# Kernel tuning notes

Measured on AMD Instinct MI355X. Metric: run time of the kernel, lower is better.

Reference implementation:

```python
import jax, jax.numpy as jnp
import numpy as np

EMBED = 8192      # DYNAMIC(2048) + STATIC(6144)
U0, U1 = 1024, 256  # units
EGO = 3
NUM_HEAD = 6
ACTION = 2
MEAN_SCALE = 5.0
INIT_STD = 5.0
MIN_STD = 1e-4
BATCH = 8192


def setup_inputs() -> dict:
    key = jax.random.key(0)
    ks = jax.random.split(key, 10)
    s = lambda fan_in: 1.0 / np.sqrt(fan_in)
    x = jax.random.normal(ks[0], (BATCH, EMBED), dtype=jnp.float32)
    # command head index in [0, 6) == RoadOption.value - 1
    command = jax.random.randint(ks[1], (BATCH,), 0, NUM_HEAD, dtype=jnp.int32)
    ego_state = jax.random.normal(ks[2], (BATCH, EGO), dtype=jnp.float32)
    # shared trunk fc: Linear(EMBED -> U0)
    fc_W = jax.random.uniform(ks[3], (EMBED, U0), jnp.float32, -s(EMBED), s(EMBED))
    fc_b = jax.random.uniform(ks[4], (U0,), jnp.float32, -s(EMBED), s(EMBED))
    # per-head MLP: Linear(U0+EGO -> U1) -> ReLU -> Linear(U1 -> 2*ACTION)
    cin = U0 + EGO
    W1 = jax.random.uniform(ks[5], (NUM_HEAD, cin, U1), jnp.float32, -s(cin), s(cin))
    b1 = jax.random.uniform(ks[6], (NUM_HEAD, U1), jnp.float32, -s(cin), s(cin))
    W2 = jax.random.uniform(ks[7], (NUM_HEAD, U1, 2 * ACTION), jnp.float32, -s(U1), s(U1))
    b2 = jax.random.uniform(ks[8], (NUM_HEAD, 2 * ACTION), jnp.float32, -s(U1), s(U1))
    return {"x": x, "command": command, "ego_state": ego_state,
            "fc_W": fc_W, "fc_b": fc_b, "W1": W1, "b1": b1, "W2": W2, "b2": b2}


def reference(x, command, ego_state, fc_W, fc_b, W1, b1, W2, b2):
    # shared trunk: Linear + ReLU, then concat ego state -> [B, U0+EGO]
    h = jax.nn.relu(x @ fc_W + fc_b)
    h = jnp.concatenate([h, ego_state], axis=-1)
    # routed heads: compute all 6 small heads densely, then select per sample
    # (faithful math; an optimized kernel would gather->grouped GEMM->scatter)
    h1 = jax.nn.relu(jnp.einsum('bi,hio->bho', h, W1) + b1)          # [B, H, U1]
    h2 = jnp.einsum('bhi,hio->bho', h1, W2) + b2                      # [B, H, 2A]
    sel = jnp.take_along_axis(h2, command[:, None, None].astype(jnp.int32), axis=1)
    out = sel[:, 0, :]                                                # [B, 2A]
    mean, std = jnp.split(out, 2, axis=-1)
    mean = MEAN_SCALE * jnp.tanh(mean / MEAN_SCALE)
    raw_init_std = np.float32(np.log(np.exp(INIT_STD) - 1.0))
    std = jax.nn.softplus(std + raw_init_std) + MIN_STD
    # distribution parameters (pre TanhBijector Normal params)
    return jnp.concatenate([mean, std], axis=-1)
```

## Files before the change

kernel.cpp:

```cpp
#include <hip/hip_runtime.h>
#include <stdint.h>

typedef short bf16x8 __attribute__((ext_vector_type(8)));
typedef float f32x4 __attribute__((ext_vector_type(4)));

#define BATCH 8192
#define EMBED 8192
#define U0    1024
#define U1    256
#define NHEAD 6

__device__ __forceinline__ unsigned short f2bf(float f) {
  union { float f; unsigned int u; } v; v.f = f;
  unsigned int u = v.u;
  unsigned int r = u + 0x7FFFu + ((u >> 16) & 1u);
  return (unsigned short)(r >> 16);
}
__device__ __forceinline__ unsigned int pk2(float lo, float hi) {
  return (unsigned int)f2bf(lo) | ((unsigned int)f2bf(hi) << 16);
}
__device__ __forceinline__ void async_copy16(const void* g, void* l) {
  __builtin_amdgcn_global_load_lds((const __attribute__((address_space(1))) void*)g,
                                   (__attribute__((address_space(3))) void*)l, 16, 0, 0);
}

__global__ void cvt_x_kernel(const float* __restrict__ x, unsigned short* __restrict__ xb) {
  long i = ((long)blockIdx.x * 256 + threadIdx.x) * 8;
  float4 a = *(const float4*)(x + i);
  float4 b = *(const float4*)(x + i + 4);
  uint4 r;
  r.x = pk2(a.x, a.y); r.y = pk2(a.z, a.w);
  r.z = pk2(b.x, b.y); r.w = pk2(b.z, b.w);
  *(uint4*)(xb + i) = r;
}

__global__ void transpose_cvt_kernel(const float* __restrict__ in, unsigned short* __restrict__ out,
                                     int R, int C, long in_z, long out_z) {
  __shared__ unsigned short tile[64][65];
  const float* inp = in + (long)blockIdx.z * in_z;
  unsigned short* outp = out + (long)blockIdx.z * out_z;
  int r0 = blockIdx.x * 64;
  int c0 = blockIdx.y * 64;
  int lc = threadIdx.x & 63;
  int lr = threadIdx.x >> 6;
#pragma unroll
  for (int i = 0; i < 16; i++) {
    int r = lr + i * 4;
    tile[r][lc] = f2bf(inp[(long)(r0 + r) * C + (c0 + lc)]);
  }
  __syncthreads();
#pragma unroll
  for (int i = 0; i < 16; i++) {
    int c = lr + i * 4;
    outp[(long)(c0 + c) * R + (r0 + lc)] = tile[lc][c];
  }
}

__global__ void bucket_kernel(const int* __restrict__ cmd, int* __restrict__ idxlist,
                              int* __restrict__ meta) {
  __shared__ int cnt[NHEAD], cur[NHEAD], off[NHEAD + 1];
  int tid = threadIdx.x;
  int lane = tid & 63;
  if (tid < NHEAD) cnt[tid] = 0;
  __syncthreads();
  for (int b = tid; b < BATCH; b += 1024) {
    int c = cmd[b];
#pragma unroll
    for (int h2 = 0; h2 < NHEAD; h2++) {
      unsigned long long m = __ballot(c == h2);
      if (lane == 0 && m) atomicAdd(&cnt[h2], __popcll(m));
    }
  }
  __syncthreads();
  if (tid == 0) {
    int s = 0;
    for (int h2 = 0; h2 < NHEAD; h2++) { off[h2] = s; s += cnt[h2]; }
    off[NHEAD] = s;
  }
  __syncthreads();
  if (tid < NHEAD) cur[tid] = off[tid];
  if (tid <= NHEAD) meta[tid] = off[tid];
  __syncthreads();
  for (int b = tid; b < BATCH; b += 1024) {
    int c = cmd[b];
#pragma unroll
    for (int h2 = 0; h2 < NHEAD; h2++) {
      unsigned long long m = __ballot(c == h2);
      int mypos = __popcll(m & ((1ull << lane) - 1ull));
      int base = 0;
      if (lane == 0 && m) base = atomicAdd(&cur[h2], __popcll(m));
      base = __shfl(base, 0);
      if (c == h2) idxlist[base + mypos] = b;
    }
  }
}

__global__ __launch_bounds__(256, 4) void gemm_kernel(const unsigned short* __restrict__ xb,
                                                      const unsigned short* __restrict__ wt,
                                                      const float* __restrict__ fc_b,
                                                      unsigned short* __restrict__ h) {
  __shared__ uint4 As[1024];
  __shared__ uint4 Bs[512];
  int tid  = threadIdx.x;
  int lane = tid & 63;
  int wave = tid >> 6;
  int wm = wave >> 1, wn = wave & 1;
  int m0 = blockIdx.x * 128;
  int n0 = blockIdx.y * 64;
  int l15 = lane & 15, lq = lane >> 4;

  long asrc[4];
#pragma unroll
  for (int j = 0; j < 4; j++) {
    int c = wave * 4 + j;
    int cwm = c >> 3, cks = (c >> 2) & 1, cmi = c & 3;
    asrc[j] = (long)(m0 + cwm * 64 + cmi * 16 + l15) * EMBED + cks * 32 + lq * 8;
  }
  long bsrc[2];
#pragma unroll
  for (int j = 0; j < 2; j++) {
    int c = wave * 2 + j;
    int cwn = c >> 2, cks = (c >> 1) & 1, cni = c & 1;
    bsrc[j] = (long)(n0 + cwn * 32 + cni * 16 + l15) * EMBED + cks * 32 + lq * 8;
  }

  f32x4 zero = {0.f, 0.f, 0.f, 0.f};
  f32x4 acc[4][2];
#pragma unroll
  for (int mi = 0; mi < 4; mi++)
#pragma unroll
    for (int ni = 0; ni < 2; ni++) acc[mi][ni] = zero;

  for (int k0 = 0; k0 < EMBED; k0 += 64) {
    __syncthreads();
#pragma unroll
    for (int j = 0; j < 4; j++) {
      int c = wave * 4 + j;
      async_copy16(xb + asrc[j] + k0, &As[c * 64 + lane]);
    }
#pragma unroll
    for (int j = 0; j < 2; j++) {
      int c = wave * 2 + j;
      async_copy16(wt + bsrc[j] + k0, &Bs[c * 64 + lane]);
    }
    __syncthreads();
#pragma unroll
    for (int ks = 0; ks < 2; ks++) {
      bf16x8 af[4], bfr[2];
#pragma unroll
      for (int mi = 0; mi < 4; mi++) af[mi] = *(const bf16x8*)&As[((wm * 2 + ks) * 4 + mi) * 64 + lane];
#pragma unroll
      for (int ni = 0; ni < 2; ni++) bfr[ni] = *(const bf16x8*)&Bs[((wn * 2 + ks) * 2 + ni) * 64 + lane];
#pragma unroll
      for (int mi = 0; mi < 4; mi++)
#pragma unroll
        for (int ni = 0; ni < 2; ni++)
          acc[mi][ni] = __builtin_amdgcn_mfma_f32_16x16x32_bf16(af[mi], bfr[ni], acc[mi][ni], 0, 0, 0);
    }
  }

#pragma unroll
  for (int ni = 0; ni < 2; ni++) {
    int col = n0 + wn * 32 + ni * 16 + l15;
    float bias = fc_b[col];
#pragma unroll
    for (int mi = 0; mi < 4; mi++) {
      int rbase = m0 + wm * 64 + mi * 16 + lq * 4;
#pragma unroll
      for (int r = 0; r < 4; r++) {
        float v = acc[mi][ni][r] + bias;
        v = v > 0.f ? v : 0.f;
        h[(long)(rbase + r) * U0 + col] = f2bf(v);
      }
    }
  }
}

__global__ __launch_bounds__(256) void head_kernel(const unsigned short* __restrict__ h,
                                                   const unsigned short* __restrict__ w1t,
                                                   const float* __restrict__ W1,
                                                   const float* __restrict__ b1,
                                                   const float* __restrict__ W2,
                                                   const float* __restrict__ b2,
                                                   const float* __restrict__ ego,
                                                   const int* __restrict__ idxlist,
                                                   const int* __restrict__ meta,
                                                   float* __restrict__ out) {
  int hd = blockIdx.y;
  int off = meta[hd];
  int cnt = meta[hd + 1] - off;
  int t0 = blockIdx.x * 32;
  if (t0 >= cnt) return;

  __shared__ int ridx[32];
  __shared__ float h1s[32][257];
  int tid = threadIdx.x;
  if (tid < 32) {
    int i = t0 + tid;
    ridx[tid] = idxlist[off + (i < cnt ? i : 0)];
  }
  __syncthreads();

  int lane = tid & 63, wave = tid >> 6;
  int l15 = lane & 15, lq = lane >> 4;

  long abase[2];
#pragma unroll
  for (int mi = 0; mi < 2; mi++) abase[mi] = (long)ridx[mi * 16 + l15] * U0 + lq * 8;
  long bbase[4];
#pragma unroll
  for (int ni = 0; ni < 4; ni++)
    bbase[ni] = (long)(hd * 256 + wave * 64 + ni * 16 + l15) * 1024 + lq * 8;

  f32x4 zero = {0.f, 0.f, 0.f, 0.f};
  f32x4 acc[2][4];
#pragma unroll
  for (int mi = 0; mi < 2; mi++)
#pragma unroll
    for (int ni = 0; ni < 4; ni++) acc[mi][ni] = zero;

#pragma unroll 2
  for (int k0 = 0; k0 < 1024; k0 += 32) {
    bf16x8 af[2], bfr[4];
#pragma unroll
    for (int mi = 0; mi < 2; mi++) af[mi] = *(const bf16x8*)(h + abase[mi] + k0);
#pragma unroll
    for (int ni = 0; ni < 4; ni++) bfr[ni] = *(const bf16x8*)(w1t + bbase[ni] + k0);
#pragma unroll
    for (int mi = 0; mi < 2; mi++)
#pragma unroll
      for (int ni = 0; ni < 4; ni++)
        acc[mi][ni] = __builtin_amdgcn_mfma_f32_16x16x32_bf16(af[mi], bfr[ni], acc[mi][ni], 0, 0, 0);
  }

  const float* W1e = W1 + (long)hd * 1027 * 256 + (long)1024 * 256;
#pragma unroll
  for (int mi = 0; mi < 2; mi++)
#pragma unroll
    for (int r = 0; r < 4; r++) {
      int rl = mi * 16 + lq * 4 + r;
      int b = ridx[rl];
      float e0 = ego[b * 3 + 0], e1 = ego[b * 3 + 1], e2 = ego[b * 3 + 2];
#pragma unroll
      for (int ni = 0; ni < 4; ni++) {
        int col = wave * 64 + ni * 16 + l15;
        float v = acc[mi][ni][r] + b1[hd * 256 + col]
                + e0 * W1e[col] + e1 * W1e[256 + col] + e2 * W1e[512 + col];
        h1s[rl][col] = v > 0.f ? v : 0.f;
      }
    }
  __syncthreads();

  if (tid < 128) {
    int t = tid >> 2, o2 = tid & 3;
    if (t0 + t < cnt) {
      const float* w2 = W2 + (long)hd * 256 * 4;
      float sum = b2[hd * 4 + o2];
      for (int i = 0; i < 256; i++) sum += h1s[t][i] * w2[i * 4 + o2];
      int b = ridx[t];
      float res;
      if (o2 < 2) {
        res = 5.0f * tanhf(sum * 0.2f);
      } else {
        float z = sum + 4.99323838f;
        res = (z > 20.f ? z : log1pf(expf(z))) + 1e-4f;
      }
      out[b * 4 + o2] = res;
    }
  }
}

extern "C" void kernel_launch(void* const* d_in, const int* in_sizes, int n_in,
                              void* d_out, int out_size, void* d_ws, size_t ws_size,
                              hipStream_t stream) {
  const float* x   = (const float*)d_in[0];
  const int*   cmd = (const int*)d_in[1];
  const float* ego = (const float*)d_in[2];
  const float* fcW = (const float*)d_in[3];
  const float* fcb = (const float*)d_in[4];
  const float* W1  = (const float*)d_in[5];
  const float* b1  = (const float*)d_in[6];
  const float* W2  = (const float*)d_in[7];
  const float* b2  = (const float*)d_in[8];
  float* out = (float*)d_out;

  char* ws = (char*)d_ws;
  unsigned short* xb   = (unsigned short*)(ws);
  unsigned short* wt   = (unsigned short*)(ws + 134217728);
  unsigned short* hbuf = (unsigned short*)(ws + 150994944);
  unsigned short* w1t  = (unsigned short*)(ws + 167772160);
  int* idxlist         = (int*)(ws + 170917888);
  int* meta            = (int*)(ws + 170950656);

  hipLaunchKernelGGL(cvt_x_kernel, dim3(32768), dim3(256), 0, stream, x, xb);
  hipLaunchKernelGGL(transpose_cvt_kernel, dim3(128, 16, 1), dim3(256), 0, stream,
                     fcW, wt, 8192, 1024, 0L, 0L);
  hipLaunchKernelGGL(transpose_cvt_kernel, dim3(16, 4, 6), dim3(256), 0, stream,
                     W1, w1t, 1024, 256, (long)1027 * 256, (long)256 * 1024);
  hipLaunchKernelGGL(bucket_kernel, dim3(1), dim3(1024), 0, stream, cmd, idxlist, meta);
  hipLaunchKernelGGL(gemm_kernel, dim3(64, 16), dim3(256), 0, stream, xb, wt, fcb, hbuf);
  hipLaunchKernelGGL(head_kernel, dim3(256, 6), dim3(256), 0, stream,
                     hbuf, w1t, W1, b1, W2, b2, ego, idxlist, meta, out);
}
```

Before: 895.6 us.

## Split-K trunk GEMM with larger 128x128 tiles and register-prefetched double buffering

Replaces the 128x64-tile trunk GEMM that used direct global-to-LDS async copies with a 128x128-tile split-K kernel (two K halves). It prefetches the next K slice into registers while the MFMAs run on the current one, and writes bf16 partial sums. A new combine kernel adds the two partials, applies the bias and ReLU, and writes h. The larger tile raises operand reuse and the split keeps the grid at 1024 blocks. In exchange it writes and reads an extra 32MB of partials, adds a launch, and rounds each partial to bf16 before the sum, which can lose precision.

```diff
diff --git a/kernel.cpp b/kernel.cpp
--- a/kernel.cpp
+++ b/kernel.cpp
@@ -19,9 +19,11 @@
 __device__ __forceinline__ unsigned int pk2(float lo, float hi) {
   return (unsigned int)f2bf(lo) | ((unsigned int)f2bf(hi) << 16);
 }
-__device__ __forceinline__ void async_copy16(const void* g, void* l) {
-  __builtin_amdgcn_global_load_lds((const __attribute__((address_space(1))) void*)g,
-                                   (__attribute__((address_space(3))) void*)l, 16, 0, 0);
+__device__ __forceinline__ float bflo(unsigned int u) {
+  union { unsigned int u; float f; } v; v.u = u << 16; return v.f;
+}
+__device__ __forceinline__ float bfhi(unsigned int u) {
+  union { unsigned int u; float f; } v; v.u = u & 0xFFFF0000u; return v.f;
 }
 
 __global__ void cvt_x_kernel(const float* __restrict__ x, unsigned short* __restrict__ xb) {
@@ -95,85 +97,118 @@
   }
 }
 
-__global__ __launch_bounds__(256, 4) void gemm_kernel(const unsigned short* __restrict__ xb,
-                                                      const unsigned short* __restrict__ wt,
-                                                      const float* __restrict__ fc_b,
-                                                      unsigned short* __restrict__ h) {
+__global__ __launch_bounds__(256, 3) void gemm_splitk_kernel(const unsigned short* __restrict__ xb,
+                                                             const unsigned short* __restrict__ wt,
+                                                             unsigned short* __restrict__ P) {
   __shared__ uint4 As[1024];
-  __shared__ uint4 Bs[512];
+  __shared__ uint4 Bs[1024];
   int tid  = threadIdx.x;
   int lane = tid & 63;
   int wave = tid >> 6;
   int wm = wave >> 1, wn = wave & 1;
   int m0 = blockIdx.x * 128;
-  int n0 = blockIdx.y * 64;
+  int n0 = blockIdx.y * 128;
+  long kbase = (long)blockIdx.z * (EMBED / 2);
+  unsigned short* pp = P + (long)blockIdx.z * BATCH * U0;
   int l15 = lane & 15, lq = lane >> 4;
 
-  long asrc[4];
+  int rloc = tid >> 3;
+  int kc   = tid & 7;
+  long ga[4], gb[4];
+  int  ld[4];
 #pragma unroll
   for (int j = 0; j < 4; j++) {
-    int c = wave * 4 + j;
-    int cwm = c >> 3, cks = (c >> 2) & 1, cmi = c & 3;
-    asrc[j] = (long)(m0 + cwm * 64 + cmi * 16 + l15) * EMBED + cks * 32 + lq * 8;
-  }
-  long bsrc[2];
-#pragma unroll
-  for (int j = 0; j < 2; j++) {
-    int c = wave * 2 + j;
-    int cwn = c >> 2, cks = (c >> 1) & 1, cni = c & 1;
-    bsrc[j] = (long)(n0 + cwn * 32 + cni * 16 + l15) * EMBED + cks * 32 + lq * 8;
+    int r = rloc + 32 * j;
+    ga[j] = (long)(m0 + r) * EMBED + kbase + kc * 8;
+    gb[j] = (long)(n0 + r) * EMBED + kbase + kc * 8;
+    int c = ((r >> 6) * 2 + (kc >> 2)) * 4 + ((r >> 4) & 3);
+    ld[j] = c * 64 + (r & 15) + 16 * (kc & 3);
   }
 
   f32x4 zero = {0.f, 0.f, 0.f, 0.f};
-  f32x4 acc[4][2];
+  f32x4 acc[4][4];
 #pragma unroll
   for (int mi = 0; mi < 4; mi++)
 #pragma unroll
-    for (int ni = 0; ni < 2; ni++) acc[mi][ni] = zero;
-
-  for (int k0 = 0; k0 < EMBED; k0 += 64) {
+    for (int ni = 0; ni < 4; ni++) acc[mi][ni] = zero;
+
+  uint4 ra[4], rb[4];
+#pragma unroll
+  for (int j = 0; j < 4; j++) {
+    ra[j] = *(const uint4*)(xb + ga[j]);
+    rb[j] = *(const uint4*)(wt + gb[j]);
+    ga[j] += 64; gb[j] += 64;
+  }
+
+  const int NSTEP = (EMBED / 2) / 64;
+  for (int k = 0; k < NSTEP; k++) {
+#pragma unroll
+    for (int j = 0; j < 4; j++) {
+      As[ld[j]] = ra[j];
+      Bs[ld[j]] = rb[j];
+    }
     __syncthreads();
-#pragma unroll
-    for (int j = 0; j < 4; j++) {
-      int c = wave * 4 + j;
-      async_copy16(xb + asrc[j] + k0, &As[c * 64 + lane]);
-    }
-#pragma unroll
-    for (int j = 0; j < 2; j++) {
-      int c = wave * 2 + j;
-      async_copy16(wt + bsrc[j] + k0, &Bs[c * 64 + lane]);
+    if (k + 1 < NSTEP) {
+#pragma unroll
+      for (int j = 0; j < 4; j++) {
+        ra[j] = *(const uint4*)(xb + ga[j]);
+        rb[j] = *(const uint4*)(wt + gb[j]);
+        ga[j] += 64; gb[j] += 64;
+      }
+    }
+#pragma unroll
+    for (int ks = 0; ks < 2; ks++) {
+      bf16x8 af[4], bfr[4];
+#pragma unroll
+      for (int mi = 0; mi < 4; mi++) af[mi] = *(const bf16x8*)&As[((wm * 2 + ks) * 4 + mi) * 64 + lane];
+#pragma unroll
+      for (int ni = 0; ni < 4; ni++) bfr[ni] = *(const bf16x8*)&Bs[((wn * 2 + ks) * 4 + ni) * 64 + lane];
+#pragma unroll
+      for (int mi = 0; mi < 4; mi++)
+#pragma unroll
+        for (int ni = 0; ni < 4; ni++)
+          acc[mi][ni] = __builtin_amdgcn_mfma_f32_16x16x32_bf16(af[mi], bfr[ni], acc[mi][ni], 0, 0, 0);
     }
     __syncthreads();
-#pragma unroll
-    for (int ks = 0; ks < 2; ks++) {
-      bf16x8 af[4], bfr[2];
-#pragma unroll
-      for (int mi = 0; mi < 4; mi++) af[mi] = *(const bf16x8*)&As[((wm * 2 + ks) * 4 + mi) * 64 + lane];
-#pragma unroll
-      for (int ni = 0; ni < 2; ni++) bfr[ni] = *(const bf16x8*)&Bs[((wn * 2 + ks) * 2 + ni) * 64 + lane];
-#pragma unroll
-      for (int mi = 0; mi < 4; mi++)
-#pragma unroll
-        for (int ni = 0; ni < 2; ni++)
-          acc[mi][ni] = __builtin_amdgcn_mfma_f32_16x16x32_bf16(af[mi], bfr[ni], acc[mi][ni], 0, 0, 0);
-    }
-  }
-
-#pragma unroll
-  for (int ni = 0; ni < 2; ni++) {
-    int col = n0 + wn * 32 + ni * 16 + l15;
-    float bias = fc_b[col];
+  }
+
+#pragma unroll
+  for (int ni = 0; ni < 4; ni++) {
+    int col = n0 + wn * 64 + ni * 16 + l15;
 #pragma unroll
     for (int mi = 0; mi < 4; mi++) {
       int rbase = m0 + wm * 64 + mi * 16 + lq * 4;
 #pragma unroll
-      for (int r = 0; r < 4; r++) {
-        float v = acc[mi][ni][r] + bias;
-        v = v > 0.f ? v : 0.f;
-        h[(long)(rbase + r) * U0 + col] = f2bf(v);
-      }
-    }
-  }
+      for (int r = 0; r < 4; r++)
+        pp[(long)(rbase + r) * U0 + col] = f2bf(acc[mi][ni][r]);
+    }
+  }
+}
+
+__global__ void combine_kernel(const unsigned short* __restrict__ P,
+                               const float* __restrict__ fc_b,
+                               unsigned short* __restrict__ h) {
+  long i = ((long)blockIdx.x * 256 + threadIdx.x) * 8;
+  uint4 a = *(const uint4*)(P + i);
+  uint4 b = *(const uint4*)(P + (long)BATCH * U0 + i);
+  int col = (int)(i & (U0 - 1));
+  float4 b0 = *(const float4*)(fc_b + col);
+  float4 b1 = *(const float4*)(fc_b + col + 4);
+  float v0 = bflo(a.x) + bflo(b.x) + b0.x;
+  float v1 = bfhi(a.x) + bfhi(b.x) + b0.y;
+  float v2 = bflo(a.y) + bflo(b.y) + b0.z;
+  float v3 = bfhi(a.y) + bfhi(b.y) + b0.w;
+  float v4 = bflo(a.z) + bflo(b.z) + b1.x;
+  float v5 = bfhi(a.z) + bfhi(b.z) + b1.y;
+  float v6 = bflo(a.w) + bflo(b.w) + b1.z;
+  float v7 = bfhi(a.w) + bfhi(b.w) + b1.w;
+  v0 = v0 > 0.f ? v0 : 0.f;  v1 = v1 > 0.f ? v1 : 0.f;
+  v2 = v2 > 0.f ? v2 : 0.f;  v3 = v3 > 0.f ? v3 : 0.f;
+  v4 = v4 > 0.f ? v4 : 0.f;  v5 = v5 > 0.f ? v5 : 0.f;
+  v6 = v6 > 0.f ? v6 : 0.f;  v7 = v7 > 0.f ? v7 : 0.f;
+  uint4 r;
+  r.x = pk2(v0, v1); r.y = pk2(v2, v3); r.z = pk2(v4, v5); r.w = pk2(v6, v7);
+  *(uint4*)(h + i) = r;
 }
 
 __global__ __launch_bounds__(256) void head_kernel(const unsigned short* __restrict__ h,
@@ -291,6 +326,7 @@
   unsigned short* w1t  = (unsigned short*)(ws + 167772160);
   int* idxlist         = (int*)(ws + 170917888);
   int* meta            = (int*)(ws + 170950656);
+  unsigned short* P    = (unsigned short*)(ws + 171048960);
 
   hipLaunchKernelGGL(cvt_x_kernel, dim3(32768), dim3(256), 0, stream, x, xb);
   hipLaunchKernelGGL(transpose_cvt_kernel, dim3(128, 16, 1), dim3(256), 0, stream,
@@ -298,7 +334,8 @@
   hipLaunchKernelGGL(transpose_cvt_kernel, dim3(16, 4, 6), dim3(256), 0, stream,
                      W1, w1t, 1024, 256, (long)1027 * 256, (long)256 * 1024);
   hipLaunchKernelGGL(bucket_kernel, dim3(1), dim3(1024), 0, stream, cmd, idxlist, meta);
-  hipLaunchKernelGGL(gemm_kernel, dim3(64, 16), dim3(256), 0, stream, xb, wt, fcb, hbuf);
+  hipLaunchKernelGGL(gemm_splitk_kernel, dim3(64, 8, 2), dim3(256), 0, stream, xb, wt, P);
+  hipLaunchKernelGGL(combine_kernel, dim3(4096), dim3(256), 0, stream, P, fcb, hbuf);
   hipLaunchKernelGGL(head_kernel, dim3(256, 6), dim3(256), 0, stream,
                      hbuf, w1t, W1, b1, W2, b2, ego, idxlist, meta, out);
 }
```

Measured after the change: 1.434 ms. 60.1% more time.
